# Kernel optimization log

Measured on AMD Instinct MI355X. Metric: run time of the kernel, lower is better.

Reference implementation:

```python
import math
import jax, jax.numpy as jnp
import numpy as np

EMB = 1024
HEADS = 16
HEAD_DIM = EMB // HEADS
FF = 4 * EMB
EPS = 1e-5


def gelu_tanh(x):
    c = math.sqrt(2.0 / math.pi)
    return 0.5 * x * (1.0 + jnp.tanh(c * (x + 0.044715 * x ** 3)))


def layernorm(x, scale, shift):
    mean = jnp.mean(x, axis=-1, keepdims=True)
    var = jnp.var(x, axis=-1, keepdims=True)
    return scale * (x - mean) / jnp.sqrt(var + EPS) + shift


def setup_inputs() -> dict:
    key = jax.random.key(0)
    ks = jax.random.split(key, 10)
    s = 0.02
    return {
        "x": jax.random.normal(ks[0], (2, 2048, EMB), dtype=jnp.float32),
        "Wq": jax.random.normal(ks[1], (EMB, EMB), dtype=jnp.float32) * s,
        "Wk": jax.random.normal(ks[2], (EMB, EMB), dtype=jnp.float32) * s,
        "Wv": jax.random.normal(ks[3], (EMB, EMB), dtype=jnp.float32) * s,
        "Wo": jax.random.normal(ks[4], (EMB, EMB), dtype=jnp.float32) * s,
        "bo": jnp.zeros((EMB,), dtype=jnp.float32),
        "W1": jax.random.normal(ks[5], (EMB, FF), dtype=jnp.float32) * s,
        "b1": jnp.zeros((FF,), dtype=jnp.float32),
        "W2": jax.random.normal(ks[6], (FF, EMB), dtype=jnp.float32) * s,
        "b2": jnp.zeros((EMB,), dtype=jnp.float32),
        "ln1_scale": jnp.ones((EMB,), dtype=jnp.float32),
        "ln1_shift": jnp.zeros((EMB,), dtype=jnp.float32),
        "ln2_scale": jnp.ones((EMB,), dtype=jnp.float32),
        "ln2_shift": jnp.zeros((EMB,), dtype=jnp.float32),
    }


def reference(x, Wq, Wk, Wv, Wo, bo, W1, b1, W2, b2,
              ln1_scale, ln1_shift, ln2_scale, ln2_shift):
    B, S, D = x.shape
    # --- pre-LN causal MHA ---
    h = layernorm(x, ln1_scale, ln1_shift)
    q = (h @ Wq).reshape(B, S, HEADS, HEAD_DIM).transpose(0, 2, 1, 3)  # [B,H,S,d]
    k = (h @ Wk).reshape(B, S, HEADS, HEAD_DIM).transpose(0, 2, 1, 3)
    v = (h @ Wv).reshape(B, S, HEADS, HEAD_DIM).transpose(0, 2, 1, 3)
    scores = jnp.einsum("bhqd,bhkd->bhqk", q, k)  # [B,H,S,S]
    causal = jnp.triu(jnp.ones((S, S), dtype=bool), k=1)
    scores = jnp.where(causal, -jnp.inf, scores)
    attn = jax.nn.softmax(scores / math.sqrt(HEAD_DIM), axis=-1)
    ctx = jnp.einsum("bhqk,bhkd->bhqd", attn, v)  # [B,H,S,d]
    ctx = ctx.transpose(0, 2, 1, 3).reshape(B, S, D)
    x = x + (ctx @ Wo + bo)
    # --- FFN ---
    h = layernorm(x, ln2_scale, ln2_shift)
    h = gelu_tanh(h @ W1 + b1) @ W2 + b2
    return x + h
```

## Files before the change

kernel.cpp:

```cpp
#include <hip/hip_runtime.h>
#include <hip/hip_bf16.h>
#include <math.h>

#define EMB 1024
#define HEADS 16
#define HEAD_DIM 64
#define FF_DIM 4096
#define SEQ 2048
#define BATCH 2
#define NTOK (BATCH * SEQ)
#define LN_EPS 1e-5f
#define QKV_N 3072
#define Q_PRESCALE 0.18033688011112042f

typedef __attribute__((ext_vector_type(8))) short s8v;
typedef __attribute__((ext_vector_type(4))) float f4v;

__device__ __forceinline__ unsigned short f2bf(float f) {
    union { __hip_bfloat16 h; unsigned short u; } cv;
    cv.h = __float2bfloat16(f);
    return cv.u;
}

__device__ __forceinline__ float fast_exp2(float x) {
#if __has_builtin(__builtin_amdgcn_exp2f)
    return __builtin_amdgcn_exp2f(x);
#else
    return exp2f(x);
#endif
}

__device__ __forceinline__ float gelu_f(float x) {
    const float c = 0.7978845608028654f;
    float x3 = x * x * x;
    return 0.5f * x * (1.0f + tanhf(c * (x + 0.044715f * x3)));
}

#define GLDS(gp, lp)                                                        \
    __builtin_amdgcn_global_load_lds(                                       \
        (const __attribute__((address_space(1))) void*)(gp),                \
        (__attribute__((address_space(3))) void*)(lp), 16, 0, 0)

__global__ __launch_bounds__(256) void ln_bf16_kernel(const float* __restrict__ x,
                                                      const float* __restrict__ scale,
                                                      const float* __restrict__ shift,
                                                      unsigned short* __restrict__ out) {
    int row = blockIdx.x;
    int tid = threadIdx.x;
    const float4 xv = ((const float4*)(x + (size_t)row * EMB))[tid];
    float s  = xv.x + xv.y + xv.z + xv.w;
    float ss = xv.x * xv.x + xv.y * xv.y + xv.z * xv.z + xv.w * xv.w;
    __shared__ float2 red[256];
    red[tid] = make_float2(s, ss);
    __syncthreads();
    for (int off = 128; off > 0; off >>= 1) {
        if (tid < off) {
            red[tid].x += red[tid + off].x;
            red[tid].y += red[tid + off].y;
        }
        __syncthreads();
    }
    float mean = red[0].x * (1.0f / EMB);
    float var  = red[0].y * (1.0f / EMB) - mean * mean;
    float rstd = rsqrtf(var + LN_EPS);
    float4 sc4 = ((const float4*)scale)[tid];
    float4 sh4 = ((const float4*)shift)[tid];
    ushort4 o;
    o.x = f2bf(sc4.x * (xv.x - mean) * rstd + sh4.x);
    o.y = f2bf(sc4.y * (xv.y - mean) * rstd + sh4.y);
    o.z = f2bf(sc4.z * (xv.z - mean) * rstd + sh4.z);
    o.w = f2bf(sc4.w * (xv.w - mean) * rstd + sh4.w);
    *(ushort4*)(out + (size_t)row * EMB + tid * 4) = o;
}

__device__ __forceinline__ void tconv_tile(const float* __restrict__ W,
                                           unsigned short* __restrict__ Wt,
                                           int K, int N, int bx, int by, int tid) {
    __shared__ float t[64][65];
    int n0 = bx * 64, k0 = by * 64;
#pragma unroll
    for (int it = 0; it < 4; ++it) {
        int f = tid + it * 256;
        int r = f >> 4, c = (f & 15) * 4;
        float4 w = *(const float4*)(W + (size_t)(k0 + r) * N + n0 + c);
        t[r][c] = w.x; t[r][c + 1] = w.y; t[r][c + 2] = w.z; t[r][c + 3] = w.w;
    }
    __syncthreads();
#pragma unroll
    for (int it = 0; it < 4; ++it) {
        int f = tid + it * 256;
        int rn = f >> 4, ck = (f & 15) * 4;
        ushort4 o;
        o.x = f2bf(t[ck + 0][rn]);
        o.y = f2bf(t[ck + 1][rn]);
        o.z = f2bf(t[ck + 2][rn]);
        o.w = f2bf(t[ck + 3][rn]);
        *(ushort4*)(Wt + (size_t)(n0 + rn) * K + k0 + ck) = o;
    }
}

__global__ __launch_bounds__(256) void tconv_all_kernel(
    const float* __restrict__ Wq, const float* __restrict__ Wk,
    const float* __restrict__ Wv, const float* __restrict__ Wo,
    const float* __restrict__ W1, const float* __restrict__ W2,
    unsigned short* __restrict__ Wqkv_t, unsigned short* __restrict__ Wo_t,
    unsigned short* __restrict__ W1_t, unsigned short* __restrict__ W2_t) {
    int b = blockIdx.x;
    int tid = threadIdx.x;
    if (b < 256)        tconv_tile(Wq, Wqkv_t,                      EMB, EMB,    b & 15, b >> 4, tid);
    else if (b < 512)   tconv_tile(Wk, Wqkv_t + (size_t)1024 * EMB, EMB, EMB,    (b - 256) & 15, (b - 256) >> 4, tid);
    else if (b < 768)   tconv_tile(Wv, Wqkv_t + (size_t)2048 * EMB, EMB, EMB,    (b - 512) & 15, (b - 512) >> 4, tid);
    else if (b < 1024)  tconv_tile(Wo, Wo_t,                        EMB, EMB,    (b - 768) & 15, (b - 768) >> 4, tid);
    else if (b < 2048)  tconv_tile(W1, W1_t,                        EMB, FF_DIM, (b - 1024) & 63, (b - 1024) >> 6, tid);
    else                tconv_tile(W2, W2_t,                        FF_DIM, EMB, (b - 2048) & 15, (b - 2048) >> 4, tid);
}

__global__ __launch_bounds__(256) void reduce_kernel(const float* __restrict__ p0,
                                                     const float* __restrict__ p1,
                                                     const float* __restrict__ bias,
                                                     const float* __restrict__ residual,
                                                     float* __restrict__ out) {
    size_t i4 = ((size_t)blockIdx.x * 256 + threadIdx.x) * 4;
    float4 a = *(const float4*)(p0 + i4);
    float4 b = *(const float4*)(p1 + i4);
    float4 r = *(const float4*)(residual + i4);
    int col = (int)(i4 & (EMB - 1));
    float4 bs = *(const float4*)(bias + col);
    float4 o;
    o.x = a.x + b.x + r.x + bs.x;
    o.y = a.y + b.y + r.y + bs.y;
    o.z = a.z + b.z + r.z + bs.z;
    o.w = a.w + b.w + r.w + bs.w;
    *(float4*)(out + i4) = o;
}

__global__ __launch_bounds__(256) void reduce_ln_kernel(const float* __restrict__ p0,
                                                        const float* __restrict__ p1,
                                                        const float* __restrict__ bias,
                                                        const float* __restrict__ residual,
                                                        float* __restrict__ x1,
                                                        const float* __restrict__ scale,
                                                        const float* __restrict__ shift,
                                                        unsigned short* __restrict__ out) {
    int row = blockIdx.x;
    int tid = threadIdx.x;
    size_t i4 = (size_t)row * EMB + tid * 4;
    float4 a = *(const float4*)(p0 + i4);
    float4 b = *(const float4*)(p1 + i4);
    float4 r = *(const float4*)(residual + i4);
    float4 bs = *(const float4*)(bias + tid * 4);
    float4 xv;
    xv.x = a.x + b.x + r.x + bs.x;
    xv.y = a.y + b.y + r.y + bs.y;
    xv.z = a.z + b.z + r.z + bs.z;
    xv.w = a.w + b.w + r.w + bs.w;
    *(float4*)(x1 + i4) = xv;

    float s  = xv.x + xv.y + xv.z + xv.w;
    float ss = xv.x * xv.x + xv.y * xv.y + xv.z * xv.z + xv.w * xv.w;
    __shared__ float2 red[256];
    red[tid] = make_float2(s, ss);
    __syncthreads();
    for (int off = 128; off > 0; off >>= 1) {
        if (tid < off) {
            red[tid].x += red[tid + off].x;
            red[tid].y += red[tid + off].y;
        }
        __syncthreads();
    }
    float mean = red[0].x * (1.0f / EMB);
    float var  = red[0].y * (1.0f / EMB) - mean * mean;
    float rstd = rsqrtf(var + LN_EPS);
    float4 sc4 = ((const float4*)scale)[tid];
    float4 sh4 = ((const float4*)shift)[tid];
    ushort4 o;
    o.x = f2bf(sc4.x * (xv.x - mean) * rstd + sh4.x);
    o.y = f2bf(sc4.y * (xv.y - mean) * rstd + sh4.y);
    o.z = f2bf(sc4.z * (xv.z - mean) * rstd + sh4.z);
    o.w = f2bf(sc4.w * (xv.w - mean) * rstd + sh4.w);
    *(ushort4*)(out + i4) = o;
}

__global__ __launch_bounds__(256, 2) void gemm_wide_kernel(
    const unsigned short* __restrict__ A,
    const unsigned short* __restrict__ Bt,
    unsigned short* __restrict__ Cb,
    int M, int N, int K,
    const float* __restrict__ bias,
    int do_gelu, int qkv_mode,
    unsigned short* __restrict__ vt)
{
    __shared__ short As[2][4096];
    __shared__ short Bs[2][8192];

    int tid = threadIdx.x;
    int m0 = blockIdx.y * 128;
    int n0 = blockIdx.x * 256;
    int wv = tid >> 6, lane = tid & 63;
    int wr = wv >> 1, wc = wv & 1;
    int quad = lane >> 4, ln = lane & 15;

    f4v acc[4][8];
#pragma unroll
    for (int i = 0; i < 4; ++i)
#pragma unroll
        for (int j = 0; j < 8; ++j) {
            f4v z = {0.f, 0.f, 0.f, 0.f};
            acc[i][j] = z;
        }

    size_t Kby = (size_t)K << 1;
    const char* Ag0 = (const char*)A + (size_t)(m0 + (tid & 127)) * Kby + (tid >> 7) * 16;
    const char* Bg0 = (const char*)Bt + (size_t)(n0 + tid) * Kby;

    int nIter = K >> 5;
    GLDS(Ag0, (char*)As[0] + tid * 16);
    GLDS(Ag0 + 32, (char*)As[0] + tid * 16 + 4096);
#pragma unroll
    for (int i = 0; i < 4; ++i)
        GLDS(Bg0 + i * 16, (char*)Bs[0] + tid * 16 + i * 4096);

    for (int it = 0; it < nIter; ++it) {
        __syncthreads();
        if (it + 1 < nIter) {
            int kb = (it + 1) << 6;
            char* Ad = (char*)As[(it + 1) & 1] + tid * 16;
            char* Bd = (char*)Bs[(it + 1) & 1] + tid * 16;
            GLDS(Ag0 + kb, Ad);
            GLDS(Ag0 + kb + 32, Ad + 4096);
#pragma unroll
            for (int i = 0; i < 4; ++i)
                GLDS(Bg0 + kb + i * 16, Bd + i * 4096);
        }
        const short* Ab = As[it & 1];
        const short* Bb = Bs[it & 1];
        s8v af[4], bfr[8];
#pragma unroll
        for (int i = 0; i < 4; ++i)
            af[i] = *(const s8v*)(Ab + ((size_t)quad * 128 + wr * 64 + i * 16 + ln) * 8);
#pragma unroll
        for (int j = 0; j < 8; ++j)
            bfr[j] = *(const s8v*)(Bb + ((size_t)quad * 256 + wc * 128 + j * 16 + ln) * 8);
#pragma unroll
        for (int i = 0; i < 4; ++i)
#pragma unroll
            for (int j = 0; j < 8; ++j)
                acc[i][j] = __builtin_amdgcn_mfma_f32_16x16x32_bf16(af[i], bfr[j], acc[i][j], 0, 0, 0);
    }

    int cn  = n0 + wc * 128 + ln;
    int cm0 = m0 + wr * 64 + quad * 4;

    if (qkv_mode) {
        if (n0 < 2048) {
            float sc = (n0 < 1024) ? Q_PRESCALE : 1.0f;
#pragma unroll
            for (int j = 0; j < 8; ++j) {
                int gn = cn + j * 16;
#pragma unroll
                for (int i = 0; i < 4; ++i)
#pragma unroll
                    for (int r = 0; r < 4; ++r)
                        Cb[(size_t)(cm0 + i * 16 + r) * 2048 + gn] = f2bf(acc[i][j][r] * sc);
            }
        } else {
#pragma unroll
            for (int j = 0; j < 8; ++j) {
                int gn = cn + j * 16 - 2048;
#pragma unroll
                for (int i = 0; i < 4; ++i) {
                    int gm0 = cm0 + i * 16;
                    int bb = gm0 >> 11, s0 = gm0 & 2047;
                    ushort4 pk;
                    pk.x = f2bf(acc[i][j][0]);
                    pk.y = f2bf(acc[i][j][1]);
                    pk.z = f2bf(acc[i][j][2]);
                    pk.w = f2bf(acc[i][j][3]);
                    *(ushort4*)(vt + ((size_t)bb * 1024 + gn) * SEQ + s0) = pk;
                }
            }
        }
        return;
    }

#pragma unroll
    for (int j = 0; j < 8; ++j) {
        int gn = cn + j * 16;
        float bj = bias ? bias[gn] : 0.f;
#pragma unroll
        for (int i = 0; i < 4; ++i) {
#pragma unroll
            for (int r = 0; r < 4; ++r) {
                float vv = acc[i][j][r] + bj;
                if (do_gelu) vv = gelu_f(vv);
                Cb[(size_t)(cm0 + i * 16 + r) * N + gn] = f2bf(vv);
            }
        }
    }
}

__global__ __launch_bounds__(256) void gemm_bf16_kernel(
    const unsigned short* __restrict__ A,
    const unsigned short* __restrict__ Bt,
    float* __restrict__ Cf0,
    float* __restrict__ Cf1,
    int M, int N, int K, int Klen)
{
    __shared__ short As[2][4096];
    __shared__ short Bs[2][4096];

    int tid = threadIdx.x;
    int m0 = blockIdx.y * 128;
    int n0 = blockIdx.x * 128;
    int k0 = blockIdx.z * Klen;
    float* Cf = blockIdx.z ? Cf1 : Cf0;
    int wv = tid >> 6, lane = tid & 63;
    int wr = wv >> 1, wc = wv & 1;
    int quad = lane >> 4, ln = lane & 15;

    f4v acc[4][4];
#pragma unroll
    for (int i = 0; i < 4; ++i)
#pragma unroll
        for (int j = 0; j < 4; ++j) {
            f4v z = {0.f, 0.f, 0.f, 0.f};
            acc[i][j] = z;
        }

    int r0 = tid & 127;
    size_t Kby = (size_t)K << 1;
    const char* Ag0 = (const char*)A + (size_t)(m0 + r0) * Kby + (size_t)k0 * 2 + (tid >> 7) * 16;
    const char* Bg0 = (const char*)Bt + (size_t)(n0 + r0) * Kby + (size_t)k0 * 2 + (tid >> 7) * 16;

    int nIter = Klen >> 5;
    GLDS(Ag0, (char*)As[0] + tid * 16);
    GLDS(Ag0 + 32, (char*)As[0] + tid * 16 + 4096);
    GLDS(Bg0, (char*)Bs[0] + tid * 16);
    GLDS(Bg0 + 32, (char*)Bs[0] + tid * 16 + 4096);

    for (int it = 0; it < nIter; ++it) {
        __syncthreads();
        if (it + 1 < nIter) {
            int kb = (it + 1) << 6;
            char* Ad = (char*)As[(it + 1) & 1] + tid * 16;
            char* Bd = (char*)Bs[(it + 1) & 1] + tid * 16;
            GLDS(Ag0 + kb, Ad);
            GLDS(Ag0 + kb + 32, Ad + 4096);
            GLDS(Bg0 + kb, Bd);
            GLDS(Bg0 + kb + 32, Bd + 4096);
        }
        const short* Ab = As[it & 1];
        const short* Bb = Bs[it & 1];
        s8v af[4], bfr[4];
#pragma unroll
        for (int i = 0; i < 4; ++i)
            af[i] = *(const s8v*)(Ab + ((size_t)quad * 128 + wr * 64 + i * 16 + ln) * 8);
#pragma unroll
        for (int j = 0; j < 4; ++j)
            bfr[j] = *(const s8v*)(Bb + ((size_t)quad * 128 + wc * 64 + j * 16 + ln) * 8);
#pragma unroll
        for (int i = 0; i < 4; ++i)
#pragma unroll
            for (int j = 0; j < 4; ++j)
                acc[i][j] = __builtin_amdgcn_mfma_f32_16x16x32_bf16(af[i], bfr[j], acc[i][j], 0, 0, 0);
    }

    int cn  = n0 + wc * 64 + ln;
    int cm0 = m0 + wr * 64 + quad * 4;
#pragma unroll
    for (int j = 0; j < 4; ++j) {
        int gn = cn + j * 16;
#pragma unroll
        for (int i = 0; i < 4; ++i)
#pragma unroll
            for (int r = 0; r < 4; ++r)
                Cf[(size_t)(cm0 + i * 16 + r) * N + gn] = acc[i][j][r];
    }
}

__global__ __launch_bounds__(256) void flash_attn_mfma_kernel(
    const unsigned short* __restrict__ qk,
    const unsigned short* __restrict__ vt,
    unsigned short* __restrict__ ctx)
{
    int h  = blockIdx.x;
    int qt = (int)gridDim.y - 1 - (int)blockIdx.y;
    int b  = blockIdx.z;
    int tid = threadIdx.x;
    int w = tid >> 6, lane = tid & 63;
    int quad = lane >> 4, ln = lane & 15;

    __shared__ short Kb2[2][4096];
    __shared__ short Vb2[2][4096];
    __shared__ short Ps[4][32 * 72];

    size_t qrow0 = (size_t)b * SEQ + (size_t)qt * 128;
    int wrow0 = w * 32;

    s8v qf[2][2];
#pragma unroll
    for (int mb = 0; mb < 2; ++mb)
#pragma unroll
        for (int ks = 0; ks < 2; ++ks)
            qf[mb][ks] = *(const s8v*)(qk + (qrow0 + wrow0 + mb * 16 + ln) * 2048
                                          + h * 64 + ks * 32 + quad * 8);

    float l_part[2][4];
    f4v o[2][4];
#pragma unroll
    for (int mb = 0; mb < 2; ++mb) {
#pragma unroll
        for (int r = 0; r < 4; ++r) l_part[mb][r] = 0.f;
#pragma unroll
        for (int db = 0; db < 4; ++db) {
            f4v z = {0.f, 0.f, 0.f, 0.f};
            o[mb][db] = z;
        }
    }

    const unsigned short* kb_p = qk + (size_t)b * SEQ * 2048 + 1024 + h * 64;
    const unsigned short* vb_p = vt + ((size_t)b * 1024 + h * 64) * SEQ;
    short* Pw = Ps[w];

    int rr = tid & 63;
    const unsigned short* Kg0 = kb_p + (size_t)rr * 2048 + (tid >> 6) * 8;
    const unsigned short* Vg0 = vb_p + (size_t)rr * 2048 + (tid >> 6) * 8;

    int ktn = 2 * qt + 2;
    int ktmax_w = (qt * 128 + wrow0 + 31) >> 6;

    GLDS(Kg0, (char*)Kb2[0] + tid * 16);
    GLDS(Kg0 + 32, (char*)Kb2[0] + tid * 16 + 4096);
    GLDS(Vg0, (char*)Vb2[0] + tid * 16);
    GLDS(Vg0 + 32, (char*)Vb2[0] + tid * 16 + 4096);

    for (int kt = 0; kt < ktn; ++kt) {
        __syncthreads();
        if (kt + 1 < ktn) {
            int nb_ = (kt + 1) & 1;
            const unsigned short* ks_ = Kg0 + (size_t)(kt + 1) * 64 * 2048;
            const unsigned short* vs_ = Vg0 + (kt + 1) * 64;
            GLDS(ks_, (char*)Kb2[nb_] + tid * 16);
            GLDS(ks_ + 32, (char*)Kb2[nb_] + tid * 16 + 4096);
            GLDS(vs_, (char*)Vb2[nb_] + tid * 16);
            GLDS(vs_ + 32, (char*)Vb2[nb_] + tid * 16 + 4096);
        }
        if (kt > ktmax_w) continue;

        const short* Kl = Kb2[kt & 1];
        const short* Vl = Vb2[kt & 1];

        f4v s[2][4];
#pragma unroll
        for (int mb = 0; mb < 2; ++mb)
#pragma unroll
            for (int nb = 0; nb < 4; ++nb) {
                f4v z = {0.f, 0.f, 0.f, 0.f};
                s[mb][nb] = z;
            }
#pragma unroll
        for (int ks = 0; ks < 2; ++ks)
#pragma unroll
            for (int nb = 0; nb < 4; ++nb) {
                s8v kfr = *(const s8v*)(Kl + ((size_t)(ks * 4 + quad) * 64 + nb * 16 + ln) * 8);
#pragma unroll
                for (int mb = 0; mb < 2; ++mb)
                    s[mb][nb] = __builtin_amdgcn_mfma_f32_16x16x32_bf16(qf[mb][ks], kfr, s[mb][nb], 0, 0, 0);
            }

#pragma unroll
        for (int mb = 0; mb < 2; ++mb) {
#pragma unroll
            for (int r = 0; r < 4; ++r) {
                int rloc = mb * 16 + quad * 4 + r;
                int grow = qt * 128 + wrow0 + rloc;
                float p[4];
#pragma unroll
                for (int nb = 0; nb < 4; ++nb) {
                    int key = kt * 64 + nb * 16 + ln;
                    float e = fast_exp2(s[mb][nb][r]);
                    p[nb] = (key > grow) ? 0.f : e;
                }
                l_part[mb][r] += (p[0] + p[1]) + (p[2] + p[3]);
#pragma unroll
                for (int nb = 0; nb < 4; ++nb)
                    Pw[rloc * 72 + nb * 16 + ln] = f2bf(p[nb]);
            }
        }

#pragma unroll
        for (int ks = 0; ks < 2; ++ks) {
            s8v pf[2];
#pragma unroll
            for (int mb = 0; mb < 2; ++mb)
                pf[mb] = *(const s8v*)(Pw + (mb * 16 + ln) * 72 + ks * 32 + quad * 8);
#pragma unroll
            for (int db = 0; db < 4; ++db) {
                s8v vfr = *(const s8v*)(Vl + ((size_t)(ks * 4 + quad) * 64 + db * 16 + ln) * 8);
#pragma unroll
                for (int mb = 0; mb < 2; ++mb)
                    o[mb][db] = __builtin_amdgcn_mfma_f32_16x16x32_bf16(pf[mb], vfr, o[mb][db], 0, 0, 0);
            }
        }
    }

#pragma unroll
    for (int mb = 0; mb < 2; ++mb)
#pragma unroll
        for (int r = 0; r < 4; ++r) {
            float l = l_part[mb][r];
#pragma unroll
            for (int msk = 1; msk < 16; msk <<= 1)
                l += __shfl_xor(l, msk);
            float inv = 1.0f / l;
            size_t row = qrow0 + wrow0 + mb * 16 + quad * 4 + r;
#pragma unroll
            for (int db = 0; db < 4; ++db)
                ctx[row * EMB + h * 64 + db * 16 + ln] = f2bf(o[mb][db][r] * inv);
        }
}

extern "C" void kernel_launch(void* const* d_in, const int* in_sizes, int n_in,
                              void* d_out, int out_size, void* d_ws, size_t ws_size,
                              hipStream_t stream) {
    const float* x    = (const float*)d_in[0];
    const float* Wq   = (const float*)d_in[1];
    const float* Wk   = (const float*)d_in[2];
    const float* Wv   = (const float*)d_in[3];
    const float* Wo   = (const float*)d_in[4];
    const float* bo   = (const float*)d_in[5];
    const float* W1   = (const float*)d_in[6];
    const float* b1   = (const float*)d_in[7];
    const float* W2   = (const float*)d_in[8];
    const float* b2   = (const float*)d_in[9];
    const float* ln1s = (const float*)d_in[10];
    const float* ln1b = (const float*)d_in[11];
    const float* ln2s = (const float*)d_in[12];
    const float* ln2b = (const float*)d_in[13];
    float* out = (float*)d_out;

    const size_t MiB = 1024 * 1024;
    uint8_t* w8 = (uint8_t*)d_ws;
    unsigned short* Wqkv_t = (unsigned short*)(w8);
    unsigned short* Wo_t   = (unsigned short*)(w8 +  6 * MiB);
    unsigned short* W1_t   = (unsigned short*)(w8 +  8 * MiB);
    unsigned short* W2_t   = (unsigned short*)(w8 + 16 * MiB);
    unsigned short* act_bf = (unsigned short*)(w8 + 24 * MiB);
    unsigned short* qk_bf  = (unsigned short*)(w8 + 32 * MiB);
    unsigned short* vt     = (unsigned short*)(w8 + 48 * MiB);
    float*          p0a    = (float*)(w8 + 32 * MiB);
    float*          p1a    = (float*)(w8 + 48 * MiB);
    unsigned short* u_bf   = (unsigned short*)(w8 + 32 * MiB);
    float*          x1     = (float*)(w8 + 64 * MiB);
    float*          p0b    = (float*)(w8);
    float*          p1b    = (float*)(w8 + 80 * MiB);

    tconv_all_kernel<<<3072, 256, 0, stream>>>(Wq, Wk, Wv, Wo, W1, W2,
                                               Wqkv_t, Wo_t, W1_t, W2_t);

    ln_bf16_kernel<<<NTOK, 256, 0, stream>>>(x, ln1s, ln1b, act_bf);

    gemm_wide_kernel<<<dim3(QKV_N / 256, NTOK / 128), 256, 0, stream>>>(
        act_bf, Wqkv_t, qk_bf, NTOK, QKV_N, EMB, nullptr, 0, 1, vt);

    flash_attn_mfma_kernel<<<dim3(HEADS, SEQ / 128, BATCH), 256, 0, stream>>>(qk_bf, vt, act_bf);

    gemm_bf16_kernel<<<dim3(EMB / 128, NTOK / 128, 2), 256, 0, stream>>>(
        act_bf, Wo_t, p0a, p1a, NTOK, EMB, EMB, 512);
    reduce_ln_kernel<<<NTOK, 256, 0, stream>>>(p0a, p1a, bo, x, x1, ln2s, ln2b, act_bf);

    gemm_wide_kernel<<<dim3(FF_DIM / 256, NTOK / 128), 256, 0, stream>>>(
        act_bf, W1_t, u_bf, NTOK, FF_DIM, EMB, b1, 1, 0, nullptr);

    gemm_bf16_kernel<<<dim3(EMB / 128, NTOK / 128, 2), 256, 0, stream>>>(
        u_bf, W2_t, p0b, p1b, NTOK, EMB, FF_DIM, 2048);
    reduce_kernel<<<(NTOK * EMB) / 1024, 256, 0, stream>>>(p0b, p1b, b2, x1, out);
}
```

Baseline: 472.3 us.

## Retile wide GEMM, add XCD-aware block mapping, LDS-staged epilogues, and attention tweaks

The wide GEMM drops from 128x256 to 128x128 tiles. Its epilogue now stages the tile through swizzled LDS so global stores are coalesced 16-byte writes, including the transposed V output. Both GEMMs get a 1D grid whose blocks are remapped so that neighbouring M tiles land on the same XCD, aiming for better L2 reuse. Barriers become explicit vmcnt waits plus s_barrier with sched_barrier fences. Flash attention applies the causal mask only on the diagonal tile, uses a partial vmcnt wait so prefetch overlaps compute, and reverses the q-tile order for the second batch to balance load. Smaller tiles mean more blocks and less reuse per block, and the hand-written waitcnt/barrier sequences carry correctness risk.

Measured after the change: 474.9 us. Within noise of the previous version (+0.6%).

```diff
diff --git a/kernel.cpp b/kernel.cpp
--- a/kernel.cpp
+++ b/kernel.cpp
@@ -40,6 +40,10 @@
     __builtin_amdgcn_global_load_lds(                                       \
         (const __attribute__((address_space(1))) void*)(gp),                \
         (__attribute__((address_space(3))) void*)(lp), 16, 0, 0)
+
+#define BAR()   do { __builtin_amdgcn_s_barrier(); __builtin_amdgcn_sched_barrier(0); } while (0)
+#define LGKM0() do { asm volatile("s_waitcnt lgkmcnt(0)" ::: "memory"); __builtin_amdgcn_sched_barrier(0); } while (0)
+#define VMCNT(n) do { asm volatile("s_waitcnt vmcnt(" #n ")" ::: "memory"); __builtin_amdgcn_sched_barrier(0); } while (0)
 
 __global__ __launch_bounds__(256) void ln_bf16_kernel(const float* __restrict__ x,
                                                       const float* __restrict__ scale,
@@ -181,7 +185,7 @@
     *(ushort4*)(out + i4) = o;
 }
 
-__global__ __launch_bounds__(256, 2) void gemm_wide_kernel(
+__global__ __launch_bounds__(256) void gemm_fused_kernel(
     const unsigned short* __restrict__ A,
     const unsigned short* __restrict__ Bt,
     unsigned short* __restrict__ Cb,
@@ -190,112 +194,131 @@
     int do_gelu, int qkv_mode,
     unsigned short* __restrict__ vt)
 {
-    __shared__ short As[2][4096];
-    __shared__ short Bs[2][8192];
+    __shared__ short lds[16384];
+    short* As = lds;
+    short* Bs = lds + 8192;
 
     int tid = threadIdx.x;
-    int m0 = blockIdx.y * 128;
-    int n0 = blockIdx.x * 256;
+    int nbx = N >> 7, nby8 = (M >> 7) >> 3;
+    int bid = (int)blockIdx.x;
+    int xcd = bid & 7;
+    int t   = bid >> 3;
+    int x   = t % nbx;
+    int u   = t / nbx;
+    int y   = (u % nby8) * 8 + xcd;
+    int m0 = y << 7, n0 = x << 7;
+
     int wv = tid >> 6, lane = tid & 63;
     int wr = wv >> 1, wc = wv & 1;
     int quad = lane >> 4, ln = lane & 15;
 
-    f4v acc[4][8];
+    f4v acc[4][4];
 #pragma unroll
     for (int i = 0; i < 4; ++i)
 #pragma unroll
-        for (int j = 0; j < 8; ++j) {
-            f4v z = {0.f, 0.f, 0.f, 0.f};
-            acc[i][j] = z;
-        }
-
+        for (int j = 0; j < 4; ++j) { f4v z4 = {0.f, 0.f, 0.f, 0.f}; acc[i][j] = z4; }
+
+    int r0 = tid & 127;
     size_t Kby = (size_t)K << 1;
-    const char* Ag0 = (const char*)A + (size_t)(m0 + (tid & 127)) * Kby + (tid >> 7) * 16;
-    const char* Bg0 = (const char*)Bt + (size_t)(n0 + tid) * Kby;
+    const char* Ag0 = (const char*)A + (size_t)(m0 + r0) * Kby + (size_t)((tid >> 7) << 4);
+    const char* Bg0 = (const char*)Bt + (size_t)(n0 + r0) * Kby + (size_t)((tid >> 7) << 4);
 
     int nIter = K >> 5;
-    GLDS(Ag0, (char*)As[0] + tid * 16);
-    GLDS(Ag0 + 32, (char*)As[0] + tid * 16 + 4096);
-#pragma unroll
-    for (int i = 0; i < 4; ++i)
-        GLDS(Bg0 + i * 16, (char*)Bs[0] + tid * 16 + i * 4096);
+    GLDS(Ag0, (char*)As + tid * 16);
+    GLDS(Ag0 + 32, (char*)As + tid * 16 + 4096);
+    GLDS(Bg0, (char*)Bs + tid * 16);
+    GLDS(Bg0 + 32, (char*)Bs + tid * 16 + 4096);
 
     for (int it = 0; it < nIter; ++it) {
-        __syncthreads();
+        VMCNT(0);
+        BAR();
         if (it + 1 < nIter) {
             int kb = (it + 1) << 6;
-            char* Ad = (char*)As[(it + 1) & 1] + tid * 16;
-            char* Bd = (char*)Bs[(it + 1) & 1] + tid * 16;
+            char* Ad = (char*)As + ((it + 1) & 1) * 8192 + tid * 16;
+            char* Bd = (char*)Bs + ((it + 1) & 1) * 8192 + tid * 16;
             GLDS(Ag0 + kb, Ad);
             GLDS(Ag0 + kb + 32, Ad + 4096);
-#pragma unroll
-            for (int i = 0; i < 4; ++i)
-                GLDS(Bg0 + kb + i * 16, Bd + i * 4096);
-        }
-        const short* Ab = As[it & 1];
-        const short* Bb = Bs[it & 1];
-        s8v af[4], bfr[8];
+            GLDS(Bg0 + kb, Bd);
+            GLDS(Bg0 + kb + 32, Bd + 4096);
+            __builtin_amdgcn_sched_barrier(0);
+        }
+        const short* Ab = As + (it & 1) * 4096;
+        const short* Bb = Bs + (it & 1) * 4096;
+        s8v af[4], bfr[4];
 #pragma unroll
         for (int i = 0; i < 4; ++i)
             af[i] = *(const s8v*)(Ab + ((size_t)quad * 128 + wr * 64 + i * 16 + ln) * 8);
 #pragma unroll
-        for (int j = 0; j < 8; ++j)
-            bfr[j] = *(const s8v*)(Bb + ((size_t)quad * 256 + wc * 128 + j * 16 + ln) * 8);
+        for (int j = 0; j < 4; ++j)
+            bfr[j] = *(const s8v*)(Bb + ((size_t)quad * 128 + wc * 64 + j * 16 + ln) * 8);
 #pragma unroll
         for (int i = 0; i < 4; ++i)
 #pragma unroll
-            for (int j = 0; j < 8; ++j)
+            for (int j = 0; j < 4; ++j)
                 acc[i][j] = __builtin_amdgcn_mfma_f32_16x16x32_bf16(af[i], bfr[j], acc[i][j], 0, 0, 0);
     }
 
-    int cn  = n0 + wc * 128 + ln;
-    int cm0 = m0 + wr * 64 + quad * 4;
-
-    if (qkv_mode) {
-        if (n0 < 2048) {
-            float sc = (n0 < 1024) ? Q_PRESCALE : 1.0f;
-#pragma unroll
-            for (int j = 0; j < 8; ++j) {
-                int gn = cn + j * 16;
-#pragma unroll
-                for (int i = 0; i < 4; ++i)
-#pragma unroll
-                    for (int r = 0; r < 4; ++r)
-                        Cb[(size_t)(cm0 + i * 16 + r) * 2048 + gn] = f2bf(acc[i][j][r] * sc);
+    LGKM0();
+    BAR();
+
+    int colb = wc * 64 + ln;
+    int rowb = wr * 64 + quad * 4;
+    int off8 = (tid & 15) * 8;
+    int sub  = tid >> 4;
+
+    if (qkv_mode && n0 >= 2048) {
+#pragma unroll
+        for (int j = 0; j < 4; ++j) {
+            int c = colb + j * 16;
+            int swz = (c & 7) << 3;
+#pragma unroll
+            for (int i = 0; i < 4; ++i) {
+                int rw = rowb + i * 16;
+                ushort4 pk;
+                pk.x = f2bf(acc[i][j][0]);
+                pk.y = f2bf(acc[i][j][1]);
+                pk.z = f2bf(acc[i][j][2]);
+                pk.w = f2bf(acc[i][j][3]);
+                *(ushort4*)(lds + c * 128 + (rw ^ swz)) = pk;
             }
-        } else {
-#pragma unroll
-            for (int j = 0; j < 8; ++j) {
-                int gn = cn + j * 16 - 2048;
-#pragma unroll
-                for (int i = 0; i < 4; ++i) {
-                    int gm0 = cm0 + i * 16;
-                    int bb = gm0 >> 11, s0 = gm0 & 2047;
-                    ushort4 pk;
-                    pk.x = f2bf(acc[i][j][0]);
-                    pk.y = f2bf(acc[i][j][1]);
-                    pk.z = f2bf(acc[i][j][2]);
-                    pk.w = f2bf(acc[i][j][3]);
-                    *(ushort4*)(vt + ((size_t)bb * 1024 + gn) * SEQ + s0) = pk;
-                }
+        }
+        BAR();
+        int bb = m0 >> 11, s0b = m0 & 2047;
+        size_t vbase = ((size_t)bb * 1024 + (n0 - 2048)) * SEQ + s0b + off8;
+#pragma unroll
+        for (int pass = 0; pass < 8; ++pass) {
+            int c = pass * 16 + sub;
+            s8v v = *(const s8v*)(lds + c * 128 + (off8 ^ ((c & 7) << 3)));
+            *(s8v*)(vt + vbase + (size_t)c * SEQ) = v;
+        }
+        return;
+    }
+
+    bool isq = qkv_mode && (n0 < 1024);
+#pragma unroll
+    for (int j = 0; j < 4; ++j) {
+        int c = colb + j * 16;
+        float bj = (!qkv_mode && bias) ? bias[n0 + c] : 0.f;
+#pragma unroll
+        for (int i = 0; i < 4; ++i) {
+            int rw = rowb + i * 16;
+#pragma unroll
+            for (int r = 0; r < 4; ++r) {
+                float vv = acc[i][j][r];
+                if (qkv_mode) { if (isq) vv *= Q_PRESCALE; }
+                else { vv += bj; if (do_gelu) vv = gelu_f(vv); }
+                int rr_ = rw + r;
+                lds[rr_ * 128 + (c ^ ((rr_ & 7) << 3))] = (short)f2bf(vv);
             }
         }
-        return;
-    }
-
-#pragma unroll
-    for (int j = 0; j < 8; ++j) {
-        int gn = cn + j * 16;
-        float bj = bias ? bias[gn] : 0.f;
-#pragma unroll
-        for (int i = 0; i < 4; ++i) {
-#pragma unroll
-            for (int r = 0; r < 4; ++r) {
-                float vv = acc[i][j][r] + bj;
-                if (do_gelu) vv = gelu_f(vv);
-                Cb[(size_t)(cm0 + i * 16 + r) * N + gn] = f2bf(vv);
-            }
-        }
+    }
+    BAR();
+    int ldc = qkv_mode ? 2048 : N;
+#pragma unroll
+    for (int pass = 0; pass < 8; ++pass) {
+        int rw = pass * 16 + sub;
+        s8v v = *(const s8v*)(lds + rw * 128 + (off8 ^ ((rw & 7) << 3)));
+        *(s8v*)(Cb + (size_t)(m0 + rw) * ldc + n0 + off8) = v;
     }
 }
 
@@ -310,10 +333,19 @@
     __shared__ short Bs[2][4096];
 
     int tid = threadIdx.x;
-    int m0 = blockIdx.y * 128;
-    int n0 = blockIdx.x * 128;
-    int k0 = blockIdx.z * Klen;
-    float* Cf = blockIdx.z ? Cf1 : Cf0;
+    int nbx = N >> 7, nby8 = (M >> 7) >> 3;
+    int bid = (int)blockIdx.x;
+    int xcd = bid & 7;
+    int t   = bid >> 3;
+    int x   = t % nbx;
+    int u   = t / nbx;
+    int y   = (u % nby8) * 8 + xcd;
+    int z   = u / nby8;
+
+    int m0 = y << 7;
+    int n0 = x << 7;
+    int k0 = z * Klen;
+    float* Cf = z ? Cf1 : Cf0;
     int wv = tid >> 6, lane = tid & 63;
     int wr = wv >> 1, wc = wv & 1;
     int quad = lane >> 4, ln = lane & 15;
@@ -323,8 +355,8 @@
     for (int i = 0; i < 4; ++i)
 #pragma unroll
         for (int j = 0; j < 4; ++j) {
-            f4v z = {0.f, 0.f, 0.f, 0.f};
-            acc[i][j] = z;
+            f4v z4 = {0.f, 0.f, 0.f, 0.f};
+            acc[i][j] = z4;
         }
 
     int r0 = tid & 127;
@@ -339,7 +371,8 @@
     GLDS(Bg0 + 32, (char*)Bs[0] + tid * 16 + 4096);
 
     for (int it = 0; it < nIter; ++it) {
-        __syncthreads();
+        VMCNT(0);
+        BAR();
         if (it + 1 < nIter) {
             int kb = (it + 1) << 6;
             char* Ad = (char*)As[(it + 1) & 1] + tid * 16;
@@ -348,6 +381,7 @@
             GLDS(Ag0 + kb + 32, Ad + 4096);
             GLDS(Bg0 + kb, Bd);
             GLDS(Bg0 + kb + 32, Bd + 4096);
+            __builtin_amdgcn_sched_barrier(0);
         }
         const short* Ab = As[it & 1];
         const short* Bb = Bs[it & 1];
@@ -384,8 +418,8 @@
     unsigned short* __restrict__ ctx)
 {
     int h  = blockIdx.x;
-    int qt = (int)gridDim.y - 1 - (int)blockIdx.y;
     int b  = blockIdx.z;
+    int qt = b ? (int)blockIdx.y : ((int)gridDim.y - 1 - (int)blockIdx.y);
     int tid = threadIdx.x;
     int w = tid >> 6, lane = tid & 63;
     int quad = lane >> 4, ln = lane & 15;
@@ -435,8 +469,9 @@
     GLDS(Vg0 + 32, (char*)Vb2[0] + tid * 16 + 4096);
 
     for (int kt = 0; kt < ktn; ++kt) {
-        __syncthreads();
-        if (kt + 1 < ktn) {
+        BAR();
+        bool pf = (kt + 1 < ktn);
+        if (pf) {
             int nb_ = (kt + 1) & 1;
             const unsigned short* ks_ = Kg0 + (size_t)(kt + 1) * 64 * 2048;
             const unsigned short* vs_ = Vg0 + (kt + 1) * 64;
@@ -446,6 +481,7 @@
             GLDS(vs_ + 32, (char*)Vb2[nb_] + tid * 16 + 4096);
         }
         if (kt > ktmax_w) continue;
+        if (pf) { VMCNT(8); } else { VMCNT(0); }
 
         const short* Kl = Kb2[kt & 1];
         const short* Vl = Vb2[kt & 1];
@@ -468,18 +504,25 @@
                     s[mb][nb] = __builtin_amdgcn_mfma_f32_16x16x32_bf16(qf[mb][ks], kfr, s[mb][nb], 0, 0, 0);
             }
 
+        bool edge = (kt == ktmax_w);
 #pragma unroll
         for (int mb = 0; mb < 2; ++mb) {
 #pragma unroll
             for (int r = 0; r < 4; ++r) {
                 int rloc = mb * 16 + quad * 4 + r;
-                int grow = qt * 128 + wrow0 + rloc;
                 float p[4];
-#pragma unroll
-                for (int nb = 0; nb < 4; ++nb) {
-                    int key = kt * 64 + nb * 16 + ln;
-                    float e = fast_exp2(s[mb][nb][r]);
-                    p[nb] = (key > grow) ? 0.f : e;
+                if (!edge) {
+#pragma unroll
+                    for (int nb = 0; nb < 4; ++nb)
+                        p[nb] = fast_exp2(s[mb][nb][r]);
+                } else {
+                    int grow = qt * 128 + wrow0 + rloc;
+#pragma unroll
+                    for (int nb = 0; nb < 4; ++nb) {
+                        int key = kt * 64 + nb * 16 + ln;
+                        float e = fast_exp2(s[mb][nb][r]);
+                        p[nb] = (key > grow) ? 0.f : e;
+                    }
                 }
                 l_part[mb][r] += (p[0] + p[1]) + (p[2] + p[3]);
 #pragma unroll
@@ -490,19 +533,21 @@
 
 #pragma unroll
         for (int ks = 0; ks < 2; ++ks) {
-            s8v pf[2];
+            s8v pf_[2];
 #pragma unroll
             for (int mb = 0; mb < 2; ++mb)
-                pf[mb] = *(const s8v*)(Pw + (mb * 16 + ln) * 72 + ks * 32 + quad * 8);
+                pf_[mb] = *(const s8v*)(Pw + (mb * 16 + ln) * 72 + ks * 32 + quad * 8);
 #pragma unroll
             for (int db = 0; db < 4; ++db) {
                 s8v vfr = *(const s8v*)(Vl + ((size_t)(ks * 4 + quad) * 64 + db * 16 + ln) * 8);
 #pragma unroll
                 for (int mb = 0; mb < 2; ++mb)
-                    o[mb][db] = __builtin_amdgcn_mfma_f32_16x16x32_bf16(pf[mb], vfr, o[mb][db], 0, 0, 0);
+                    o[mb][db] = __builtin_amdgcn_mfma_f32_16x16x32_bf16(pf_[mb], vfr, o[mb][db], 0, 0, 0);
             }
         }
     }
+
+    asm volatile("s_waitcnt vmcnt(0)" ::: "memory");
 
 #pragma unroll
     for (int mb = 0; mb < 2; ++mb)
@@ -560,19 +605,19 @@
 
     ln_bf16_kernel<<<NTOK, 256, 0, stream>>>(x, ln1s, ln1b, act_bf);
 
-    gemm_wide_kernel<<<dim3(QKV_N / 256, NTOK / 128), 256, 0, stream>>>(
+    gemm_fused_kernel<<<(NTOK / 128) * (QKV_N / 128), 256, 0, stream>>>(
         act_bf, Wqkv_t, qk_bf, NTOK, QKV_N, EMB, nullptr, 0, 1, vt);
 
     flash_attn_mfma_kernel<<<dim3(HEADS, SEQ / 128, BATCH), 256, 0, stream>>>(qk_bf, vt, act_bf);
 
-    gemm_bf16_kernel<<<dim3(EMB / 128, NTOK / 128, 2), 256, 0, stream>>>(
+    gemm_bf16_kernel<<<(EMB / 128) * (NTOK / 128) * 2, 256, 0, stream>>>(
         act_bf, Wo_t, p0a, p1a, NTOK, EMB, EMB, 512);
     reduce_ln_kernel<<<NTOK, 256, 0, stream>>>(p0a, p1a, bo, x, x1, ln2s, ln2b, act_bf);
 
-    gemm_wide_kernel<<<dim3(FF_DIM / 256, NTOK / 128), 256, 0, stream>>>(
+    gemm_fused_kernel<<<(NTOK / 128) * (FF_DIM / 128), 256, 0, stream>>>(
         act_bf, W1_t, u_bf, NTOK, FF_DIM, EMB, b1, 1, 0, nullptr);
 
-    gemm_bf16_kernel<<<dim3(EMB / 128, NTOK / 128, 2), 256, 0, stream>>>(
+    gemm_bf16_kernel<<<(EMB / 128) * (NTOK / 128) * 2, 256, 0, stream>>>(
         u_bf, W2_t, p0b, p1b, NTOK, EMB, FF_DIM, 2048);
     reduce_kernel<<<(NTOK * EMB) / 1024, 256, 0, stream>>>(p0b, p1b, b2, x1, out);
 }
```
